# Optimization experiments

Measured on AMD Instinct MI355X. Metric: run time of the kernel, lower is better.

## Reference

```python
import jax, jax.numpy as jnp
import numpy as np

SCALE = 4  # fft branch asserts scale == 4


def setup_inputs() -> dict:
    key = jax.random.key(0)
    B, T, D = 1, 131072, 128
    x = jax.random.normal(key, (B, T, D), dtype=jnp.float32)
    return {"x": x}


def reference(x):
    """Sliding-window 4-point FFT pooling (real part).

    For each position i the torch code takes segment
    x[:, max(0, i-1) : min(i+3, T), :], right-pads it with zeros to
    length 4, FFTs along the window axis, keeps the real part.
    coarse = mean over window axis -> [1, T, D]
    fine   = windows flattened     -> [1, T, 4*D]
    """
    B, T, D = x.shape
    S = SCALE
    i = jnp.arange(T)[:, None]            # [T, 1]
    j = jnp.arange(S)[None, :]            # [1, S]
    start = jnp.maximum(0, i - 1)         # left edge of window
    pos = start + j                       # candidate source index [T, S]
    # valid iff pos < i+3 (window end) and pos < T (sequence end);
    # invalid slots are the right zero-padding of the torch code.
    mask = (pos < i + 3) & (pos < T)
    idx = jnp.clip(pos, 0, T - 1)
    windows = x[:, idx, :] * mask[None, :, :, None].astype(x.dtype)  # [B,T,S,D]
    wf = jnp.fft.fft(windows, axis=2).real.astype(x.dtype)           # [B,T,S,D]
    coarse = wf.mean(axis=2)              # [B, T, D]
    fine = wf.reshape(1, T, S * D)        # [1, T, S*D]
    return coarse, fine
```

## Files before the change

kernel.cpp:

```cpp
#include <hip/hip_runtime.h>


__global__ __launch_bounds__(256) void pool_fft_kernel(
    const float* __restrict__ x,
    float* __restrict__ coarse,
    float* __restrict__ fine,
    int T) {
    const int gtid = blockIdx.x * blockDim.x + threadIdx.x;
    const int lane = gtid & 31;
    const int i = gtid >> 5;
    if (i >= T) return;
    const int d4 = lane << 2;

    const int start = (i == 0) ? 0 : (i - 1);
    const int nvalid = (i == 0) ? 3 : min(4, T - start);

    float4 w0 = make_float4(0.f, 0.f, 0.f, 0.f);
    float4 w1 = w0, w2 = w0, w3 = w0;

    const float* base = x + (size_t)start * 128 + d4;
    w0 = *reinterpret_cast<const float4*>(base);
    w1 = *reinterpret_cast<const float4*>(base + 128);
    if (nvalid > 2) w2 = *reinterpret_cast<const float4*>(base + 256);
    if (nvalid > 3) w3 = *reinterpret_cast<const float4*>(base + 384);

    *reinterpret_cast<float4*>(&coarse[(size_t)i * 128 + d4]) = w0;

    float4 f0, f1, f2;
    f0.x = w0.x + w1.x + w2.x + w3.x;
    f0.y = w0.y + w1.y + w2.y + w3.y;
    f0.z = w0.z + w1.z + w2.z + w3.z;
    f0.w = w0.w + w1.w + w2.w + w3.w;
    f1.x = w0.x - w2.x;
    f1.y = w0.y - w2.y;
    f1.z = w0.z - w2.z;
    f1.w = w0.w - w2.w;
    f2.x = w0.x - w1.x + w2.x - w3.x;
    f2.y = w0.y - w1.y + w2.y - w3.y;
    f2.z = w0.z - w1.z + w2.z - w3.z;
    f2.w = w0.w - w1.w + w2.w - w3.w;

    float* fb = fine + (size_t)i * 512 + d4;
    *reinterpret_cast<float4*>(fb)       = f0;
    *reinterpret_cast<float4*>(fb + 128) = f1;
    *reinterpret_cast<float4*>(fb + 256) = f2;
    *reinterpret_cast<float4*>(fb + 384) = f1;
}

extern "C" void kernel_launch(void* const* d_in, const int* in_sizes, int n_in,
                              void* d_out, int out_size, void* d_ws, size_t ws_size,
                              hipStream_t stream) {
    const float* x = (const float*)d_in[0];
    const int D = 128;
    const int T = in_sizes[0] / D;
    float* coarse = (float*)d_out;
    float* fine = (float*)d_out + (size_t)T * D;

    const int threads_per_row = D / 4;
    const long long total = (long long)T * threads_per_row;
    const int block = 256;
    const int grid = (int)((total + block - 1) / block);
    pool_fft_kernel<<<grid, block, 0, stream>>>(x, coarse, fine, T);
}
```

Measured before the change: 375.2 us.

## Process two adjacent windows per thread and use nontemporal stores

Each thread now handles two consecutive output positions, loading five input rows instead of eight and reusing the shared rows across both windows. Output stores become nontemporal to avoid polluting cache with write-only data. This halves the thread count and assumes T is even, since an odd final row would not be written.

```diff
diff --git a/kernel.cpp b/kernel.cpp
--- a/kernel.cpp
+++ b/kernel.cpp
@@ -1,50 +1,63 @@
 #include <hip/hip_runtime.h>
 
 
-__global__ __launch_bounds__(256) void pool_fft_kernel(
+typedef float f4 __attribute__((ext_vector_type(4)));
+
+__device__ __forceinline__ f4 ldf4(const float* p) {
+    return *reinterpret_cast<const f4*>(p);
+}
+
+__device__ __forceinline__ void emit_window(
+    float* __restrict__ coarse, float* __restrict__ fine,
+    long long i, int d4,
+    f4 w0, f4 w1, f4 w2, f4 w3) {
+    f4 f0 = w0 + w1 + w2 + w3;
+    f4 f1 = w0 - w2;
+    f4 f2 = w0 - w1 + w2 - w3;
+    __builtin_nontemporal_store(w0, reinterpret_cast<f4*>(coarse + i * 128 + d4));
+    float* fb = fine + i * 512 + d4;
+    __builtin_nontemporal_store(f0, reinterpret_cast<f4*>(fb));
+    __builtin_nontemporal_store(f1, reinterpret_cast<f4*>(fb + 128));
+    __builtin_nontemporal_store(f2, reinterpret_cast<f4*>(fb + 256));
+    __builtin_nontemporal_store(f1, reinterpret_cast<f4*>(fb + 384));
+}
+
+__global__ __launch_bounds__(256) void pool_fft2_kernel(
     const float* __restrict__ x,
     float* __restrict__ coarse,
     float* __restrict__ fine,
     int T) {
     const int gtid = blockIdx.x * blockDim.x + threadIdx.x;
     const int lane = gtid & 31;
-    const int i = gtid >> 5;
-    if (i >= T) return;
+    const int p = gtid >> 5;
+    const int P = T >> 1;
+    if (p >= P) return;
+    const int i0 = p << 1;
     const int d4 = lane << 2;
+    const f4 Z = {0.f, 0.f, 0.f, 0.f};
 
-    const int start = (i == 0) ? 0 : (i - 1);
-    const int nvalid = (i == 0) ? 3 : min(4, T - start);
-
-    float4 w0 = make_float4(0.f, 0.f, 0.f, 0.f);
-    float4 w1 = w0, w2 = w0, w3 = w0;
-
-    const float* base = x + (size_t)start * 128 + d4;
-    w0 = *reinterpret_cast<const float4*>(base);
-    w1 = *reinterpret_cast<const float4*>(base + 128);
-    if (nvalid > 2) w2 = *reinterpret_cast<const float4*>(base + 256);
-    if (nvalid > 3) w3 = *reinterpret_cast<const float4*>(base + 384);
-
-    *reinterpret_cast<float4*>(&coarse[(size_t)i * 128 + d4]) = w0;
-
-    float4 f0, f1, f2;
-    f0.x = w0.x + w1.x + w2.x + w3.x;
-    f0.y = w0.y + w1.y + w2.y + w3.y;
-    f0.z = w0.z + w1.z + w2.z + w3.z;
-    f0.w = w0.w + w1.w + w2.w + w3.w;
-    f1.x = w0.x - w2.x;
-    f1.y = w0.y - w2.y;
-    f1.z = w0.z - w2.z;
-    f1.w = w0.w - w2.w;
-    f2.x = w0.x - w1.x + w2.x - w3.x;
-    f2.y = w0.y - w1.y + w2.y - w3.y;
-    f2.z = w0.z - w1.z + w2.z - w3.z;
-    f2.w = w0.w - w1.w + w2.w - w3.w;
-
-    float* fb = fine + (size_t)i * 512 + d4;
-    *reinterpret_cast<float4*>(fb)       = f0;
-    *reinterpret_cast<float4*>(fb + 128) = f1;
-    *reinterpret_cast<float4*>(fb + 256) = f2;
-    *reinterpret_cast<float4*>(fb + 384) = f1;
+    if (i0 == 0) {
+        const float* b = x + d4;
+        f4 A  = ldf4(b);
+        f4 B  = ldf4(b + 128);
+        f4 C  = ldf4(b + 256);
+        f4 Dv = ldf4(b + 384);
+        emit_window(coarse, fine, 0, d4, A, B, C, Z);
+        emit_window(coarse, fine, 1, d4, A, B, C, Dv);
+    } else {
+        const float* b = x + (size_t)(i0 - 1) * 128 + d4;
+        f4 L0 = ldf4(b);
+        f4 L1 = ldf4(b + 128);
+        f4 L2 = ldf4(b + 256);
+        const int r3 = min(i0 + 2, T - 1);
+        const int r4 = min(i0 + 3, T - 1);
+        f4 L3 = ldf4(x + (size_t)r3 * 128 + d4);
+        f4 L4 = ldf4(x + (size_t)r4 * 128 + d4);
+        if (i0 + 2 >= T) L3 = Z;
+        if (i0 + 3 >= T) L4 = Z;
+        emit_window(coarse, fine, i0,     d4, L0, L1, L2, L3);
+        emit_window(coarse, fine, i0 + 1, d4, L1, L2, L3, L4);
+    }
 }
 
 extern "C" void kernel_launch(void* const* d_in, const int* in_sizes, int n_in,
@@ -56,9 +69,9 @@
     float* coarse = (float*)d_out;
     float* fine = (float*)d_out + (size_t)T * D;
 
-    const int threads_per_row = D / 4;
-    const long long total = (long long)T * threads_per_row;
+    const long long pairs = T / 2;
+    const long long total = pairs * 32;
     const int block = 256;
     const int grid = (int)((total + block - 1) / block);
-    pool_fft_kernel<<<grid, block, 0, stream>>>(x, coarse, fine, T);
+    pool_fft2_kernel<<<grid, block, 0, stream>>>(x, coarse, fine, T);
 }
```

Measured after the change: 366.2 us. -2.4%, faster.

## Process four rows per wave with register reuse and nontemporal stores

Applied to the files above, without the earlier changes.

Each 64-lane wave now handles four consecutive output rows. It loads the seven overlapping input rows once into registers instead of re-reading four rows per output row. The two half-waves split the FFT outputs and the coarse writes between them, so each lane issues fewer and wider coalesced stores. Output stores use nontemporal hints to avoid polluting the cache with write-only data. Boundary handling for the first and last rows now relies on clamped loads and select logic, which adds some instruction overhead.

```diff
diff --git a/kernel.cpp b/kernel.cpp
--- a/kernel.cpp
+++ b/kernel.cpp
@@ -1,50 +1,59 @@
 #include <hip/hip_runtime.h>
 
 
-__global__ __launch_bounds__(256) void pool_fft_kernel(
+typedef float f4 __attribute__((ext_vector_type(4)));
+
+__device__ __forceinline__ f4 ldf4(const float* p) {
+    return *reinterpret_cast<const f4*>(p);
+}
+
+__global__ __launch_bounds__(256) void pool_fft4_kernel(
     const float* __restrict__ x,
     float* __restrict__ coarse,
     float* __restrict__ fine,
     int T) {
-    const int gtid = blockIdx.x * blockDim.x + threadIdx.x;
-    const int lane = gtid & 31;
-    const int i = gtid >> 5;
-    if (i >= T) return;
-    const int d4 = lane << 2;
+    const int wv   = threadIdx.x >> 6;
+    const int lane = threadIdx.x & 63;
+    const int half = lane >> 5;
+    const int c    = lane & 31;
+    const int d4   = c << 2;
+    const int r0   = (blockIdx.x * 4 + wv) * 4;
+    if (r0 >= T) return;
 
-    const int start = (i == 0) ? 0 : (i - 1);
-    const int nvalid = (i == 0) ? 3 : min(4, T - start);
+    const f4 Z = {0.f, 0.f, 0.f, 0.f};
 
-    float4 w0 = make_float4(0.f, 0.f, 0.f, 0.f);
-    float4 w1 = w0, w2 = w0, w3 = w0;
+    f4 t[7];
+#pragma unroll
+    for (int k = 0; k < 7; ++k) {
+        const int row = r0 - 1 + k;
+        const int rc  = min(max(row, 0), T - 1);
+        const f4 v = ldf4(x + (size_t)rc * 128 + d4);
+        t[k] = (row >= T) ? Z : v;
+    }
 
-    const float* base = x + (size_t)start * 128 + d4;
-    w0 = *reinterpret_cast<const float4*>(base);
-    w1 = *reinterpret_cast<const float4*>(base + 128);
-    if (nvalid > 2) w2 = *reinterpret_cast<const float4*>(base + 256);
-    if (nvalid > 3) w3 = *reinterpret_cast<const float4*>(base + 384);
+    {
+        const f4 cA = half ? t[1] : ((r0 == 0) ? t[1] : t[0]);
+        const f4 cB = half ? t[3] : t[2];
+        __builtin_nontemporal_store(
+            cA, reinterpret_cast<f4*>(coarse + (size_t)(r0 + half) * 128 + d4));
+        __builtin_nontemporal_store(
+            cB, reinterpret_cast<f4*>(coarse + (size_t)(r0 + 2 + half) * 128 + d4));
+    }
 
-    *reinterpret_cast<float4*>(&coarse[(size_t)i * 128 + d4]) = w0;
-
-    float4 f0, f1, f2;
-    f0.x = w0.x + w1.x + w2.x + w3.x;
-    f0.y = w0.y + w1.y + w2.y + w3.y;
-    f0.z = w0.z + w1.z + w2.z + w3.z;
-    f0.w = w0.w + w1.w + w2.w + w3.w;
-    f1.x = w0.x - w2.x;
-    f1.y = w0.y - w2.y;
-    f1.z = w0.z - w2.z;
-    f1.w = w0.w - w2.w;
-    f2.x = w0.x - w1.x + w2.x - w3.x;
-    f2.y = w0.y - w1.y + w2.y - w3.y;
-    f2.z = w0.z - w1.z + w2.z - w3.z;
-    f2.w = w0.w - w1.w + w2.w - w3.w;
-
-    float* fb = fine + (size_t)i * 512 + d4;
-    *reinterpret_cast<float4*>(fb)       = f0;
-    *reinterpret_cast<float4*>(fb + 128) = f1;
-    *reinterpret_cast<float4*>(fb + 256) = f2;
-    *reinterpret_cast<float4*>(fb + 384) = f1;
+#pragma unroll
+    for (int q = 0; q < 4; ++q) {
+        const int i = r0 + q;
+        f4 w0 = t[q], w1 = t[q + 1], w2 = t[q + 2], w3 = t[q + 3];
+        if (q == 0 && r0 == 0) {
+            w0 = t[1]; w1 = t[2]; w2 = t[3]; w3 = Z;
+        }
+        const f4 f1 = w0 - w2;
+        const f4 vA = half ? f1 : (w0 + w1 + w2 + w3);
+        const f4 vB = half ? f1 : (w0 - w1 + w2 - w3);
+        float* fb = fine + (size_t)i * 512 + half * 128 + d4;
+        __builtin_nontemporal_store(vA, reinterpret_cast<f4*>(fb));
+        __builtin_nontemporal_store(vB, reinterpret_cast<f4*>(fb + 256));
+    }
 }
 
 extern "C" void kernel_launch(void* const* d_in, const int* in_sizes, int n_in,
@@ -56,9 +65,7 @@
     float* coarse = (float*)d_out;
     float* fine = (float*)d_out + (size_t)T * D;
 
-    const int threads_per_row = D / 4;
-    const long long total = (long long)T * threads_per_row;
-    const int block = 256;
-    const int grid = (int)((total + block - 1) / block);
-    pool_fft_kernel<<<grid, block, 0, stream>>>(x, coarse, fine, T);
+    const int rows_per_block = 16;
+    const int grid = (T + rows_per_block - 1) / rows_per_block;
+    pool_fft4_kernel<<<grid, 256, 0, stream>>>(x, coarse, fine, T);
 }
```

Measured after the change: 363.1 us. 3.2% less time.
